# Performance work log

Hardware: AMD Instinct MI355X
Metric: run time of the kernel (lower is better)

## Reference

```python
import jax, jax.numpy as jnp
import numpy as np

N, NQ, M, DQ, DK, DV, H = 4, 512, 512, 256, 256, 256, 256


def setup_inputs() -> dict:
    key = jax.random.key(0)
    ks = jax.random.split(key, 6)
    scale_q = 1.0 / np.sqrt(DQ)
    scale_k = 1.0 / np.sqrt(DK)
    scale_v = 1.0 / np.sqrt(H)
    return {
        "query": jax.random.normal(ks[0], (N, NQ, DQ), jnp.float32),
        "key": jax.random.normal(ks[1], (N, M, DK), jnp.float32),
        "value": jax.random.normal(ks[2], (N, M, DV), jnp.float32),
        "W_q": jax.random.normal(ks[3], (DQ, H), jnp.float32) * scale_q,
        "W_k": jax.random.normal(ks[4], (DK, H), jnp.float32) * scale_k,
        "W_v": jax.random.normal(ks[5], (H,), jnp.float32) * scale_v,
    }


def reference(query, key, value, W_q, W_k, W_v):
    # project: (N, n, H) and (N, m, H)
    q = jnp.einsum("bnd,dh->bnh", query, W_q)
    k = jnp.einsum("bmd,dh->bmh", key, W_k)
    # broadcast add -> (N, n, m, H), tanh, project H->1 -> scores (N, n, m)
    scores = jnp.einsum("bnmh,h->bnm", jnp.tanh(q[:, :, None, :] + k[:, None, :, :]), W_v)
    attn = jax.nn.softmax(scores, axis=-1)  # (N, n, m)
    return jnp.einsum("bnm,bmv->bnv", attn, value)
```

## Files before the change

### kernel.cpp

```cpp
#include <hip/hip_runtime.h>

#define NB 4
#define NQL 512
#define ML 512
#define DDIM 256
#define HDIM 256

static constexpr float TWO_LOG2E = 2.8853900817779268f;
static constexpr float LOG2E     = 1.4426950408889634f;

#define SB() __builtin_amdgcn_sched_barrier(0)

#define PJ_LOAD(Xr, Wr, c)                                          \
    {                                                               \
        const int d_ = (c) * 4;                                     \
        Xr[0] = *(const float4*)(xr0 + d_);                         \
        Xr[1] = *(const float4*)(xr1 + d_);                         \
        Xr[2] = *(const float4*)(xr2 + d_);                         \
        Xr[3] = *(const float4*)(xr3 + d_);                         \
        Wr[0] = *(const float4*)(wc + (size_t)(d_ + 0) * HDIM);     \
        Wr[1] = *(const float4*)(wc + (size_t)(d_ + 1) * HDIM);     \
        Wr[2] = *(const float4*)(wc + (size_t)(d_ + 2) * HDIM);     \
        Wr[3] = *(const float4*)(wc + (size_t)(d_ + 3) * HDIM);     \
    }

#define PJ_FMA(Xr, Wr, i, comp, r)                                  \
    acc[i][0] = fmaf(Xr[i].comp, Wr[r].x, acc[i][0]);               \
    acc[i][1] = fmaf(Xr[i].comp, Wr[r].y, acc[i][1]);               \
    acc[i][2] = fmaf(Xr[i].comp, Wr[r].z, acc[i][2]);               \
    acc[i][3] = fmaf(Xr[i].comp, Wr[r].w, acc[i][3]);

#define PJ_ROW(Xr, Wr, i)                                           \
    PJ_FMA(Xr, Wr, i, x, 0) PJ_FMA(Xr, Wr, i, y, 1)                 \
    PJ_FMA(Xr, Wr, i, z, 2) PJ_FMA(Xr, Wr, i, w, 3)

#define PJ_COMP(Xr, Wr)                                             \
    PJ_ROW(Xr, Wr, 0) PJ_ROW(Xr, Wr, 1)                             \
    PJ_ROW(Xr, Wr, 2) PJ_ROW(Xr, Wr, 3)

__global__ __launch_bounds__(256) void proj_kernel(
    const float* __restrict__ q_src, const float* __restrict__ k_src,
    const float* __restrict__ Wq,    const float* __restrict__ Wk,
    float* __restrict__ EqT,         float* __restrict__ EkT)
{
    const int idx   = blockIdx.x;
    const int b     = idx & 3;
    const int which = (idx >> 2) & 1;
    const int lt    = (idx >> 3) & 7;
    const int ht    = idx >> 6;
    const float* __restrict__ src = which ? k_src : q_src;
    const float* __restrict__ W   = which ? Wk : Wq;
    float* __restrict__ outT      = which ? EkT : EqT;

    const int l0 = lt * 64, h0 = ht * 64;
    const int t  = threadIdx.x;
    const int tx = t & 15;
    const int ty = t >> 4;

    const float* xr0 = &src[(size_t)(b * NQL + l0 + ty * 4) * DDIM];
    const float* xr1 = xr0 + DDIM;
    const float* xr2 = xr0 + 2 * DDIM;
    const float* xr3 = xr0 + 3 * DDIM;
    const float* wc  = &W[h0 + tx * 4];

    float4 XA[4], WA[4], XB[4], WB[4];
    float acc[4][4] = {};

    PJ_LOAD(XA, WA, 0)
    SB();
    for (int v = 0; v < 31; ++v) {
        PJ_LOAD(XB, WB, 2 * v + 1)
        SB();
        PJ_COMP(XA, WA)
        SB();
        PJ_LOAD(XA, WA, 2 * v + 2)
        SB();
        PJ_COMP(XB, WB)
        SB();
    }
    PJ_LOAD(XB, WB, 63)
    SB();
    PJ_COMP(XA, WA)
    SB();
    PJ_COMP(XB, WB)

    #pragma unroll
    for (int j = 0; j < 4; ++j) {
        float4 o;
        o.x = __builtin_amdgcn_exp2f(acc[0][j] * TWO_LOG2E);
        o.y = __builtin_amdgcn_exp2f(acc[1][j] * TWO_LOG2E);
        o.z = __builtin_amdgcn_exp2f(acc[2][j] * TWO_LOG2E);
        o.w = __builtin_amdgcn_exp2f(acc[3][j] * TWO_LOG2E);
        *(float4*)&outT[(size_t)(b * HDIM + h0 + tx * 4 + j) * NQL + l0 + ty * 4] = o;
    }
}

__global__ __launch_bounds__(256) void scores_kernel(
    const float* __restrict__ EqT, const float* __restrict__ EkT,
    const float* __restrict__ Wv, float* __restrict__ P,
    float* __restrict__ Spart)
{
    const int idx = blockIdx.x;
    const int b   = idx & 3;
    const int mt  = (idx >> 2) & 15;
    const int nt  = idx >> 6;
    const int m0  = mt * 32, n0 = nt * 64;
    const int t   = threadIdx.x;
    const int tx  = t & 15;
    const int ty  = t >> 4;

    __shared__ float sQ[2][32][68];
    __shared__ float sK[2][32][36];

    const int rq = t >> 3, cq = t & 7;
    const int rk = t >> 3, ck = t & 7;

    const float* qbase = &EqT[(size_t)b * HDIM * NQL + n0];
    const float* kbase = &EkT[(size_t)b * HDIM * ML + m0];

    float4 q1 = *(const float4*)(qbase + (size_t)rq * NQL + cq * 8);
    float4 q2 = *(const float4*)(qbase + (size_t)rq * NQL + cq * 8 + 4);
    float4 kv = *(const float4*)(kbase + (size_t)rk * ML + ck * 4);

    float acc[4][2] = {};
    float swv = 0.f;
    int cur = 0;

    for (int c = 0; c < 8; ++c) {
        *(float4*)&sQ[cur][rq][cq * 8]     = q1;
        *(float4*)&sQ[cur][rq][cq * 8 + 4] = q2;
        *(float4*)&sK[cur][rk][ck * 4]     = kv;
        __syncthreads();
        if (c < 7) {
            const float* qn = qbase + (size_t)((c + 1) * 32 + rq) * NQL;
            q1 = *(const float4*)(qn + cq * 8);
            q2 = *(const float4*)(qn + cq * 8 + 4);
            kv = *(const float4*)(kbase + (size_t)((c + 1) * 32 + rk) * ML + ck * 4);
        }
        const float* wvp = Wv + c * 32;
        #pragma unroll 8
        for (int hh = 0; hh < 32; ++hh) {
            float4 q4 = *(const float4*)&sQ[cur][hh][ty * 4];
            float2 k2 = *(const float2*)&sK[cur][hh][tx * 2];
            const float wv = wvp[hh];
            swv += wv;
            const float nw2 = -2.0f * wv;
            {
                float a0 = fmaf(q4.x, k2.x, 1.0f);
                float a1 = fmaf(q4.y, k2.x, 1.0f);
                float a2 = fmaf(q4.z, k2.x, 1.0f);
                float a3 = fmaf(q4.w, k2.x, 1.0f);
                float r01 = __builtin_amdgcn_rcpf(a0 * a1);
                float r23 = __builtin_amdgcn_rcpf(a2 * a3);
                float t01 = nw2 * r01, t23 = nw2 * r23;
                acc[0][0] = fmaf(t01, a1, acc[0][0]);
                acc[1][0] = fmaf(t01, a0, acc[1][0]);
                acc[2][0] = fmaf(t23, a3, acc[2][0]);
                acc[3][0] = fmaf(t23, a2, acc[3][0]);
            }
            {
                float a0 = fmaf(q4.x, k2.y, 1.0f);
                float a1 = fmaf(q4.y, k2.y, 1.0f);
                float a2 = fmaf(q4.z, k2.y, 1.0f);
                float a3 = fmaf(q4.w, k2.y, 1.0f);
                float r01 = __builtin_amdgcn_rcpf(a0 * a1);
                float r23 = __builtin_amdgcn_rcpf(a2 * a3);
                float t01 = nw2 * r01, t23 = nw2 * r23;
                acc[0][1] = fmaf(t01, a1, acc[0][1]);
                acc[1][1] = fmaf(t01, a0, acc[1][1]);
                acc[2][1] = fmaf(t23, a3, acc[2][1]);
                acc[3][1] = fmaf(t23, a2, acc[3][1]);
            }
        }
        cur ^= 1;
    }

    float rs[4];
    #pragma unroll
    for (int i = 0; i < 4; ++i) {
        float2 p;
        p.x = __builtin_amdgcn_exp2f((swv + acc[i][0]) * LOG2E);
        p.y = __builtin_amdgcn_exp2f((swv + acc[i][1]) * LOG2E);
        *(float2*)&P[(size_t)(b * NQL + n0 + ty * 4 + i) * ML + m0 + tx * 2] = p;
        rs[i] = p.x + p.y;
    }
    #pragma unroll
    for (int off = 1; off < 16; off <<= 1) {
        #pragma unroll
        for (int i = 0; i < 4; ++i) rs[i] += __shfl_xor(rs[i], off);
    }
    if (tx == 0) {
        #pragma unroll
        for (int i = 0; i < 4; ++i)
            Spart[(size_t)(mt * NB + b) * NQL + n0 + ty * 4 + i] = rs[i];
    }
}

#define AV_ONE(PSb, VSb, i, r, comp)                                 \
    acc[i][0] = fmaf(PSb[i].comp, VSb[r].x, acc[i][0]);              \
    acc[i][1] = fmaf(PSb[i].comp, VSb[r].y, acc[i][1]);              \
    acc[i][2] = fmaf(PSb[i].comp, VSb[r].z, acc[i][2]);              \
    acc[i][3] = fmaf(PSb[i].comp, VSb[r].w, acc[i][3]);
#define AV_RR(PSb, VSb, r, comp)                                     \
    AV_ONE(PSb, VSb, 0, r, comp) AV_ONE(PSb, VSb, 1, r, comp)        \
    AV_ONE(PSb, VSb, 2, r, comp) AV_ONE(PSb, VSb, 3, r, comp)
#define AV_COMP(PSb, VSb)                                            \
    AV_RR(PSb, VSb, 0, x) AV_RR(PSb, VSb, 1, y)                      \
    AV_RR(PSb, VSb, 2, z) AV_RR(PSb, VSb, 3, w)

#define AV_LOAD(PSb, VSb, c)                                              \
    {                                                                     \
        const int mm_ = (c) * 4;                                          \
        _Pragma("unroll")                                                 \
        for (int r_ = 0; r_ < 4; ++r_) {                                  \
            PSb[r_] = *(const float4*)(pbase + (size_t)r_ * ML + mm_);    \
            VSb[r_] = *(const float4*)(vbase + (size_t)(mm_ + r_) * DDIM);\
        }                                                                 \
    }

__global__ __launch_bounds__(256) void av_kernel(
    const float* __restrict__ P, const float* __restrict__ Spart,
    const float* __restrict__ V, float* __restrict__ O)
{
    const int idx = blockIdx.x;
    const int b   = idx & 3;
    const int vt  = (idx >> 2) & 3;
    const int nt  = idx >> 4;
    const int v0  = vt * 64, n0 = nt * 16;
    const int t    = threadIdx.x;
    const int lane = t & 63;
    const int wid  = t >> 6;
    const int tx   = lane & 15;
    const int tn   = lane >> 4;

    __shared__ float sInv[16];
    __shared__ float sRed[3][16][64];

    if (t < 16) {
        float s = 0.f;
        #pragma unroll
        for (int mt = 0; mt < 16; ++mt)
            s += Spart[(size_t)(mt * NB + b) * NQL + n0 + t];
        sInv[t] = 1.0f / s;
    }

    const float* pbase = &P[(size_t)(b * NQL + n0 + tn * 4) * ML + wid * 128];
    const float* vbase = &V[(size_t)(b * ML + wid * 128) * DDIM + v0 + tx * 4];

    float4 PA[4], VA[4];
    float4 PB[4], VB[4];
    float acc[4][4] = {};

    AV_LOAD(PA, VA, 0)
    SB();
    for (int v = 0; v < 15; ++v) {
        AV_LOAD(PB, VB, 2 * v + 1)
        SB();
        AV_COMP(PA, VA)
        SB();
        AV_LOAD(PA, VA, 2 * v + 2)
        SB();
        AV_COMP(PB, VB)
        SB();
    }
    AV_LOAD(PB, VB, 31)
    SB();
    AV_COMP(PA, VA)
    SB();
    AV_COMP(PB, VB)

    __syncthreads();
    if (wid != 0) {
        #pragma unroll
        for (int i = 0; i < 4; ++i) {
            float4 r = {acc[i][0], acc[i][1], acc[i][2], acc[i][3]};
            *(float4*)&sRed[wid - 1][tn * 4 + i][tx * 4] = r;
        }
    }
    __syncthreads();
    if (wid == 0) {
        #pragma unroll
        for (int i = 0; i < 4; ++i) {
            float4 r1 = *(const float4*)&sRed[0][tn * 4 + i][tx * 4];
            float4 r2 = *(const float4*)&sRed[1][tn * 4 + i][tx * 4];
            float4 r3 = *(const float4*)&sRed[2][tn * 4 + i][tx * 4];
            const float inv = sInv[tn * 4 + i];
            float4 o;
            o.x = (acc[i][0] + r1.x + r2.x + r3.x) * inv;
            o.y = (acc[i][1] + r1.y + r2.y + r3.y) * inv;
            o.z = (acc[i][2] + r1.z + r2.z + r3.z) * inv;
            o.w = (acc[i][3] + r1.w + r2.w + r3.w) * inv;
            *(float4*)&O[(size_t)(b * NQL + n0 + tn * 4 + i) * DDIM + v0 + tx * 4] = o;
        }
    }
}

extern "C" void kernel_launch(void* const* d_in, const int* in_sizes, int n_in,
                              void* d_out, int out_size, void* d_ws, size_t ws_size,
                              hipStream_t stream)
{
    const float* query = (const float*)d_in[0];
    const float* key   = (const float*)d_in[1];
    const float* value = (const float*)d_in[2];
    const float* Wq    = (const float*)d_in[3];
    const float* Wk    = (const float*)d_in[4];
    const float* Wv    = (const float*)d_in[5];
    float* out = (float*)d_out;

    float* EqT   = (float*)d_ws;
    float* EkT   = EqT + (size_t)NB * HDIM * NQL;
    float* P     = EkT + (size_t)NB * HDIM * ML;
    float* Spart = P + (size_t)NB * NQL * ML;

    proj_kernel<<<dim3(256), 256, 0, stream>>>(query, key, Wq, Wk, EqT, EkT);
    scores_kernel<<<dim3(512), 256, 0, stream>>>(EqT, EkT, Wv, P, Spart);
    av_kernel<<<dim3(512), 256, 0, stream>>>(P, Spart, value, out);
}
```

Baseline: 142.9 us.

## Enlarge scores tile to 64x64 with split-H across two thread groups

The scores kernel now computes a 64x64 (n,m) tile per block of 512 threads, each thread owning a 4x4 output micro-tile instead of 4x2. The H dimension is split between two 256-thread groups, and their partial sums are combined through shared memory before the exp and row-sum step. The aim is more reuse of each shared-memory load (a float4 of K instead of a float2) and fewer blocks, which halves the Spart partials read by the AV kernel. In exchange it adds a shared-memory reduction and an extra barrier, and the second group sits idle during the epilogue. Launching 256 blocks may also reduce occupancy.

```diff
diff --git a/kernel.cpp b/kernel.cpp
--- a/kernel.cpp
+++ b/kernel.cpp
@@ -95,104 +95,110 @@
     }
 }
 
-__global__ __launch_bounds__(256) void scores_kernel(
+#define SC_M(jm, km)                                         \
+    {                                                        \
+        float a0 = fmaf(q4.x, km, 1.0f);                     \
+        float a1 = fmaf(q4.y, km, 1.0f);                     \
+        float a2 = fmaf(q4.z, km, 1.0f);                     \
+        float a3 = fmaf(q4.w, km, 1.0f);                     \
+        float r01 = __builtin_amdgcn_rcpf(a0 * a1);          \
+        float r23 = __builtin_amdgcn_rcpf(a2 * a3);          \
+        float t01 = nw2 * r01, t23 = nw2 * r23;              \
+        acc[0][jm] = fmaf(t01, a1, acc[0][jm]);              \
+        acc[1][jm] = fmaf(t01, a0, acc[1][jm]);              \
+        acc[2][jm] = fmaf(t23, a3, acc[2][jm]);              \
+        acc[3][jm] = fmaf(t23, a2, acc[3][jm]);              \
+    }
+
+__global__ __launch_bounds__(512) void scores_kernel(
     const float* __restrict__ EqT, const float* __restrict__ EkT,
     const float* __restrict__ Wv, float* __restrict__ P,
     float* __restrict__ Spart)
 {
     const int idx = blockIdx.x;
     const int b   = idx & 3;
-    const int mt  = (idx >> 2) & 15;
-    const int nt  = idx >> 6;
-    const int m0  = mt * 32, n0 = nt * 64;
-    const int t   = threadIdx.x;
-    const int tx  = t & 15;
-    const int ty  = t >> 4;
-
-    __shared__ float sQ[2][32][68];
-    __shared__ float sK[2][32][36];
-
-    const int rq = t >> 3, cq = t & 7;
-    const int rk = t >> 3, ck = t & 7;
-
-    const float* qbase = &EqT[(size_t)b * HDIM * NQL + n0];
-    const float* kbase = &EkT[(size_t)b * HDIM * ML + m0];
-
-    float4 q1 = *(const float4*)(qbase + (size_t)rq * NQL + cq * 8);
-    float4 q2 = *(const float4*)(qbase + (size_t)rq * NQL + cq * 8 + 4);
-    float4 kv = *(const float4*)(kbase + (size_t)rk * ML + ck * 4);
-
-    float acc[4][2] = {};
-    float swv = 0.f;
+    const int mt  = (idx >> 2) & 7;
+    const int nt  = idx >> 5;
+    const int m0  = mt * 64, n0 = nt * 64;
+    const int t    = threadIdx.x;
+    const int lane = t & 63;
+    const int wid  = t >> 6;
+    const int g    = wid >> 2;
+    const int tg   = (wid & 3) * 64 + lane;
+    const int tx   = tg & 15;
+    const int ty   = tg >> 4;
+
+    __shared__ float sQ[2][2][16][68];
+    __shared__ float sK[2][2][16][68];
+
+    const int rs_ = tg >> 4, cs_ = tg & 15;
+
+    const float* qbase = &EqT[(size_t)(b * HDIM + g * 128) * NQL + n0];
+    const float* kbase = &EkT[(size_t)(b * HDIM + g * 128) * ML + m0];
+
+    float4 qv = *(const float4*)(qbase + (size_t)rs_ * NQL + cs_ * 4);
+    float4 kv = *(const float4*)(kbase + (size_t)rs_ * ML + cs_ * 4);
+
+    float acc[4][4] = {};
     int cur = 0;
 
     for (int c = 0; c < 8; ++c) {
-        *(float4*)&sQ[cur][rq][cq * 8]     = q1;
-        *(float4*)&sQ[cur][rq][cq * 8 + 4] = q2;
-        *(float4*)&sK[cur][rk][ck * 4]     = kv;
+        *(float4*)&sQ[g][cur][rs_][cs_ * 4] = qv;
+        *(float4*)&sK[g][cur][rs_][cs_ * 4] = kv;
         __syncthreads();
         if (c < 7) {
-            const float* qn = qbase + (size_t)((c + 1) * 32 + rq) * NQL;
-            q1 = *(const float4*)(qn + cq * 8);
-            q2 = *(const float4*)(qn + cq * 8 + 4);
-            kv = *(const float4*)(kbase + (size_t)((c + 1) * 32 + rk) * ML + ck * 4);
-        }
-        const float* wvp = Wv + c * 32;
+            qv = *(const float4*)(qbase + (size_t)((c + 1) * 16 + rs_) * NQL + cs_ * 4);
+            kv = *(const float4*)(kbase + (size_t)((c + 1) * 16 + rs_) * ML + cs_ * 4);
+        }
+        const float* wvp = Wv + g * 128 + c * 16;
+        #pragma unroll
+        for (int hh = 0; hh < 16; ++hh) {
+            float4 q4 = *(const float4*)&sQ[g][cur][hh][ty * 4];
+            float4 k4 = *(const float4*)&sK[g][cur][hh][tx * 4];
+            const float nw2 = -2.0f * wvp[hh];
+            SC_M(0, k4.x) SC_M(1, k4.y) SC_M(2, k4.z) SC_M(3, k4.w)
+        }
+        cur ^= 1;
+    }
+
+    __syncthreads();
+    float* sred = &sQ[0][0][0][0];
+    if (g == 1) {
+        #pragma unroll
+        for (int i = 0; i < 4; ++i)
+            #pragma unroll
+            for (int j = 0; j < 4; ++j)
+                sred[(i * 4 + j) * 256 + tg] = acc[i][j];
+    }
+    __syncthreads();
+    if (g == 0) {
+        float swv = 0.f;
         #pragma unroll 8
-        for (int hh = 0; hh < 32; ++hh) {
-            float4 q4 = *(const float4*)&sQ[cur][hh][ty * 4];
-            float2 k2 = *(const float2*)&sK[cur][hh][tx * 2];
-            const float wv = wvp[hh];
-            swv += wv;
-            const float nw2 = -2.0f * wv;
-            {
-                float a0 = fmaf(q4.x, k2.x, 1.0f);
-                float a1 = fmaf(q4.y, k2.x, 1.0f);
-                float a2 = fmaf(q4.z, k2.x, 1.0f);
-                float a3 = fmaf(q4.w, k2.x, 1.0f);
-                float r01 = __builtin_amdgcn_rcpf(a0 * a1);
-                float r23 = __builtin_amdgcn_rcpf(a2 * a3);
-                float t01 = nw2 * r01, t23 = nw2 * r23;
-                acc[0][0] = fmaf(t01, a1, acc[0][0]);
-                acc[1][0] = fmaf(t01, a0, acc[1][0]);
-                acc[2][0] = fmaf(t23, a3, acc[2][0]);
-                acc[3][0] = fmaf(t23, a2, acc[3][0]);
-            }
-            {
-                float a0 = fmaf(q4.x, k2.y, 1.0f);
-                float a1 = fmaf(q4.y, k2.y, 1.0f);
-                float a2 = fmaf(q4.z, k2.y, 1.0f);
-                float a3 = fmaf(q4.w, k2.y, 1.0f);
-                float r01 = __builtin_amdgcn_rcpf(a0 * a1);
-                float r23 = __builtin_amdgcn_rcpf(a2 * a3);
-                float t01 = nw2 * r01, t23 = nw2 * r23;
-                acc[0][1] = fmaf(t01, a1, acc[0][1]);
-                acc[1][1] = fmaf(t01, a0, acc[1][1]);
-                acc[2][1] = fmaf(t23, a3, acc[2][1]);
-                acc[3][1] = fmaf(t23, a2, acc[3][1]);
-            }
-        }
-        cur ^= 1;
-    }
-
-    float rs[4];
-    #pragma unroll
-    for (int i = 0; i < 4; ++i) {
-        float2 p;
-        p.x = __builtin_amdgcn_exp2f((swv + acc[i][0]) * LOG2E);
-        p.y = __builtin_amdgcn_exp2f((swv + acc[i][1]) * LOG2E);
-        *(float2*)&P[(size_t)(b * NQL + n0 + ty * 4 + i) * ML + m0 + tx * 2] = p;
-        rs[i] = p.x + p.y;
-    }
-    #pragma unroll
-    for (int off = 1; off < 16; off <<= 1) {
-        #pragma unroll
-        for (int i = 0; i < 4; ++i) rs[i] += __shfl_xor(rs[i], off);
-    }
-    if (tx == 0) {
-        #pragma unroll
-        for (int i = 0; i < 4; ++i)
-            Spart[(size_t)(mt * NB + b) * NQL + n0 + ty * 4 + i] = rs[i];
+        for (int i = 0; i < HDIM; i += 4) {
+            float4 w = *(const float4*)(Wv + i);
+            swv += (w.x + w.y) + (w.z + w.w);
+        }
+        float rsum[4];
+        #pragma unroll
+        for (int i = 0; i < 4; ++i) {
+            float4 p;
+            p.x = __builtin_amdgcn_exp2f((swv + acc[i][0] + sred[(i * 4 + 0) * 256 + tg]) * LOG2E);
+            p.y = __builtin_amdgcn_exp2f((swv + acc[i][1] + sred[(i * 4 + 1) * 256 + tg]) * LOG2E);
+            p.z = __builtin_amdgcn_exp2f((swv + acc[i][2] + sred[(i * 4 + 2) * 256 + tg]) * LOG2E);
+            p.w = __builtin_amdgcn_exp2f((swv + acc[i][3] + sred[(i * 4 + 3) * 256 + tg]) * LOG2E);
+            *(float4*)&P[(size_t)(b * NQL + n0 + ty * 4 + i) * ML + m0 + tx * 4] = p;
+            rsum[i] = (p.x + p.y) + (p.z + p.w);
+        }
+        #pragma unroll
+        for (int off = 1; off < 16; off <<= 1) {
+            #pragma unroll
+            for (int i = 0; i < 4; ++i) rsum[i] += __shfl_xor(rsum[i], off);
+        }
+        if (tx == 0) {
+            #pragma unroll
+            for (int i = 0; i < 4; ++i)
+                Spart[(size_t)(mt * NB + b) * NQL + n0 + ty * 4 + i] = rsum[i];
+        }
     }
 }
 
@@ -239,7 +245,7 @@
     if (t < 16) {
         float s = 0.f;
         #pragma unroll
-        for (int mt = 0; mt < 16; ++mt)
+        for (int mt = 0; mt < 8; ++mt)
             s += Spart[(size_t)(mt * NB + b) * NQL + n0 + t];
         sInv[t] = 1.0f / s;
     }
@@ -313,6 +319,6 @@
     float* Spart = P + (size_t)NB * NQL * ML;
 
     proj_kernel<<<dim3(256), 256, 0, stream>>>(query, key, Wq, Wk, EqT, EkT);
-    scores_kernel<<<dim3(512), 256, 0, stream>>>(EqT, EkT, Wv, P, Spart);
+    scores_kernel<<<dim3(256), 512, 0, stream>>>(EqT, EkT, Wv, P, Spart);
     av_kernel<<<dim3(512), 256, 0, stream>>>(P, Spart, value, out);
 }
```

After: 136.8 us. 4.3% less time.
